# Optimization experiments

Hardware: AMD Instinct MI355X
Metric: run time of the kernel (lower is better)

Reference implementation:

```python
import jax, jax.numpy as jnp
import numpy as np
import math

NUM_HEADS = 16


def _alibi_slopes(num_heads: int):
    # geometric sequence for power-of-2 head counts (paper's scheme)
    def slopes_pow2(n):
        start = 2.0 ** (-(2.0 ** (-(math.log2(n) - 3))))
        return [start * (start ** i) for i in range(n)]
    if math.log2(num_heads).is_integer():
        return slopes_pow2(num_heads)
    c = 2 ** math.floor(math.log2(num_heads))
    extra = slopes_pow2(2 * c)[0::2][: num_heads - c]
    return slopes_pow2(c) + extra


def setup_inputs() -> dict:
    key = jax.random.key(0)
    kq, kk, kv = jax.random.split(key, 3)
    B, H, S, D = 2, NUM_HEADS, 2048, 64
    q = jax.random.normal(kq, (B, H, S, D), dtype=jnp.float32)
    k = jax.random.normal(kk, (B, H, S, D), dtype=jnp.float32)
    v = jax.random.normal(kv, (B, H, S, D), dtype=jnp.float32)
    return {"q": q, "k": k, "v": v}


def reference(q, k, v):
    B, H, Sq, D = q.shape
    Sk = k.shape[2]
    slopes = jnp.asarray(_alibi_slopes(H), dtype=jnp.float32)  # [H]
    pos = jnp.arange(Sk)
    # abs relative positions (symmetric, non-causal) as in the source
    rel = jnp.abs(pos[None, :] - pos[:, None]).astype(jnp.float32)  # [Sk, Sk]
    alibi = -slopes[:, None, None] * rel[None, :Sq, :]  # [H, Sq, Sk]
    scores = jnp.einsum("bhqd,bhkd->bhqk", q, k) / math.sqrt(D)
    scores = scores + alibi[None]
    probs = jax.nn.softmax(scores, axis=-1)
    return jnp.einsum("bhqk,bhkd->bhqd", probs, v)
```

## Files before the change

### kernel.cpp

```cpp
#include <hip/hip_runtime.h>
#include <hip/hip_bf16.h>
#include <math.h>

typedef __bf16 bf16;
typedef __attribute__((ext_vector_type(8))) bf16 bf16x8;
typedef __attribute__((ext_vector_type(2))) bf16 bf16x2;
typedef __attribute__((ext_vector_type(16))) float f32x16;
typedef __attribute__((ext_vector_type(4))) unsigned int uint4v;

#define SQ 2048
#define DH 64
#define NH 16
#define KVT 32
#define NKVT (SQ / KVT)
#define REC 8192
#define LOG2E 1.44269504088896340736f
#define THETA 14.0f
#define NITEMS 1024
#define GRID 1024

__device__ __forceinline__ float fast_exp2(float x) {
#if __has_builtin(__builtin_amdgcn_exp2f)
    return __builtin_amdgcn_exp2f(x);
#else
    return exp2f(x);
#endif
}

__device__ __forceinline__ unsigned pkbf16(float a, float b) {
    union { bf16x2 h; unsigned u; } x;
    x.h = (bf16x2){(bf16)a, (bf16)b};
    return x.u;
}

#if __has_builtin(__builtin_amdgcn_permlane32_swap)
__device__ __forceinline__ void plswap(unsigned &a, unsigned &b) {
    typedef __attribute__((ext_vector_type(2))) unsigned int uint2v;
    uint2v r = __builtin_amdgcn_permlane32_swap(a, b, false, false);
    a = r[0]; b = r[1];
}
#else
__device__ __forceinline__ void plswap(unsigned &a, unsigned &b) {
    asm volatile("v_permlane32_swap_b32 %0, %1" : "+v"(a), "+v"(b));
}
#endif

union FragU { uint4v u; bf16x8 b; };

__global__ __launch_bounds__(256)
void alibi_prep_kernel(const float* __restrict__ K, const float* __restrict__ V,
                       char* __restrict__ W, int* __restrict__ ctr) {
    __shared__ bf16 lt[64][80];
    const int t  = threadIdx.x;
    const int s0 = blockIdx.x * 64;
    const int bh = blockIdx.y;
    if (ctr && blockIdx.x == 0 && blockIdx.y == 0 && blockIdx.z == 0 && t == 0)
        *ctr = 0;
    if (blockIdx.z == 0) {
#pragma unroll
        for (int i = 0; i < 2; ++i) {
            const int g    = i * 256 + t;
            const int tile = g >> 8;
            const int cc   = g & 255;
            const int ds   = cc >> 6;
            const int lane = cc & 63;
            const float* p = K + ((size_t)bh * SQ + s0 + tile * 32 + (lane & 31)) * DH
                               + ds * 16 + (lane >> 5) * 8;
            float4 a = *(const float4*)p, b = *(const float4*)(p + 4);
            bf16x8 pk = {(bf16)a.x,(bf16)a.y,(bf16)a.z,(bf16)a.w,
                         (bf16)b.x,(bf16)b.y,(bf16)b.z,(bf16)b.w};
            *(bf16x8*)(W + (size_t)(bh * NKVT + (s0 >> 5) + tile) * REC
                         + ds * 1024 + lane * 16) = pk;
        }
    } else {
#pragma unroll
        for (int i = 0; i < 2; ++i) {
            int idx = i * 256 + t;
            int row = idx >> 3, c8 = idx & 7;
            const float* p = V + ((size_t)bh * SQ + s0 + row) * DH + c8 * 8;
            float4 a = *(const float4*)p, b = *(const float4*)(p + 4);
            bf16 e[8] = {(bf16)a.x,(bf16)a.y,(bf16)a.z,(bf16)a.w,
                         (bf16)b.x,(bf16)b.y,(bf16)b.z,(bf16)b.w};
#pragma unroll
            for (int jj = 0; jj < 8; ++jj) lt[c8 * 8 + jj][row] = e[jj];
        }
        __syncthreads();
#pragma unroll
        for (int i = 0; i < 2; ++i) {
            const int g    = i * 256 + t;
            const int tile = g >> 8;
            const int cc   = g & 255;
            const int grp  = cc >> 6;
            const int lane = cc & 63;
            const int d    = (grp >> 1) * 32 + (lane & 31);
            const int sv   = tile * 32 + (grp & 1) * 16 + (lane >> 5) * 8;
            bf16x8 v = *(const bf16x8*)&lt[d][sv];
            *(bf16x8*)(W + (size_t)(bh * NKVT + (s0 >> 5) + tile) * REC
                         + 4096 + grp * 1024 + lane * 16) = v;
        }
    }
}

__global__ __launch_bounds__(256, 2)
void alibi_attn_kernel(const float* __restrict__ Q, const char* __restrict__ W,
                       float* __restrict__ Out, int* __restrict__ ctr) {
    __shared__ float ex[2][64][72];
    __shared__ int s_id;
    const int tid  = threadIdx.x;
    const int lane = tid & 63;
    const int par  = tid >> 6;
    const int r32  = lane & 31;
    const int hi   = lane >> 5;
    const float QSCALE = 0.125f * LOG2E;

    int next_static = blockIdx.x;

    while (true) {
        if (tid == 0) s_id = ctr ? atomicAdd(ctr, 1) : next_static;
        __syncthreads();
        const int r = s_id;
        next_static += GRID;
        if (r >= NITEMS) break;

        const int h   = 15 - (r >> 6);
        const int sub = r & 63;
        const int bh  = (sub >> 5) * NH + h;
        const int q0  = (sub & 31) * 64;

        const float slope2  = exp2f(-0.5f * (float)(h + 1)) * LOG2E;
        const float SLOPE2N = -slope2;
        const int D = (int)(THETA / slope2);
        const int a0 = q0 - D;
        const int tmin = (a0 <= 0) ? 0 : (a0 >> 5);
        const int tmax = min(NKVT - 1, (q0 + 63 + D) >> 5);

        const float* Qp = Q + (size_t)bh * SQ * DH;
        float*       Op = Out + (size_t)bh * SQ * DH;
        const char*  rec = W + (size_t)bh * NKVT * REC;

        const int qrowA = q0 + r32;
        bf16x8 qfragA[4], qfragB[4];
#pragma unroll
        for (int ds = 0; ds < 4; ++ds) {
            const float* sa = Qp + (size_t)qrowA * DH + ds * 16 + hi * 8;
            float4 a = *(const float4*)sa, b = *(const float4*)(sa + 4);
            qfragA[ds] = (bf16x8){(bf16)(a.x*QSCALE),(bf16)(a.y*QSCALE),
                                  (bf16)(a.z*QSCALE),(bf16)(a.w*QSCALE),
                                  (bf16)(b.x*QSCALE),(bf16)(b.y*QSCALE),
                                  (bf16)(b.z*QSCALE),(bf16)(b.w*QSCALE)};
            const float* sb = sa + 32 * DH;
            float4 c = *(const float4*)sb, d = *(const float4*)(sb + 4);
            qfragB[ds] = (bf16x8){(bf16)(c.x*QSCALE),(bf16)(c.y*QSCALE),
                                  (bf16)(c.z*QSCALE),(bf16)(c.w*QSCALE),
                                  (bf16)(d.x*QSCALE),(bf16)(d.y*QSCALE),
                                  (bf16)(d.z*QSCALE),(bf16)(d.w*QSCALE)};
        }

        f32x16 oaccA[2], oaccB[2];
#pragma unroll
        for (int d2 = 0; d2 < 2; ++d2)
#pragma unroll
            for (int rr = 0; rr < 16; ++rr) { oaccA[d2][rr] = 0.f; oaccB[d2][rr] = 0.f; }
        float psA[4] = {0.f,0.f,0.f,0.f}, psB[4] = {0.f,0.f,0.f,0.f};
        const float qhA = (float)(qrowA - 4 * hi);

        auto LOADF = [&](bf16x8* kf, bf16x8* vf, int tt) {
            const char* rb = rec + (size_t)tt * REC + lane * 16;
#pragma unroll
            for (int ds = 0; ds < 4; ++ds) kf[ds] = *(const bf16x8*)(rb + ds * 1024);
#pragma unroll
            for (int g = 0; g < 4; ++g)    vf[g] = *(const bf16x8*)(rb + 4096 + g * 1024);
        };

        auto COMPUTE = [&](const bf16x8* kf, const bf16x8* vf, int tt) {
            const float gq0 = qhA - (float)(tt * KVT);
#pragma unroll
            for (int qs = 0; qs < 2; ++qs) {
                const bf16x8* qf = qs ? qfragB : qfragA;
                f32x16*       oa = qs ? oaccB  : oaccA;
                float*        ps = qs ? psB    : psA;
                const float   gq = qs ? gq0 + 32.f : gq0;

                f32x16 sacc;
#pragma unroll
                for (int rr = 0; rr < 16; ++rr) sacc[rr] = 0.f;
                __builtin_amdgcn_s_setprio(1);
#pragma unroll
                for (int ds = 0; ds < 4; ++ds)
                    sacc = __builtin_amdgcn_mfma_f32_32x32x16_bf16(kf[ds], qf[ds], sacc, 0, 0, 0);
                __builtin_amdgcn_s_setprio(0);

                float p[16];
#pragma unroll
                for (int reg = 0; reg < 16; ++reg) {
                    const int krel = (reg & 3) + 8 * (reg >> 2);
                    float d = gq - (float)krel;
                    float s2 = fmaf(SLOPE2N, fabsf(d), sacc[reg]);
                    float e = fast_exp2(s2);
                    p[reg] = e;
                    ps[reg & 3] += e;
                }

                __builtin_amdgcn_s_setprio(1);
#pragma unroll
                for (int ks = 0; ks < 2; ++ks) {
                    unsigned u0 = pkbf16(p[8 * ks + 0], p[8 * ks + 1]);
                    unsigned u1 = pkbf16(p[8 * ks + 2], p[8 * ks + 3]);
                    unsigned v0 = pkbf16(p[8 * ks + 4], p[8 * ks + 5]);
                    unsigned v1 = pkbf16(p[8 * ks + 6], p[8 * ks + 7]);
                    plswap(u0, v0);
                    plswap(u1, v1);
                    FragU pf; pf.u = (uint4v){u0, u1, v0, v1};
#pragma unroll
                    for (int dblk = 0; dblk < 2; ++dblk)
                        oa[dblk] = __builtin_amdgcn_mfma_f32_32x32x16_bf16(vf[dblk * 2 + ks], pf.b, oa[dblk], 0, 0, 0);
                }
                __builtin_amdgcn_s_setprio(0);
            }
        };

        {
            bf16x8 kA[4], vA[4], kB[4], vB[4];
            int t = tmin + par;
            if (t <= tmax) {
                const int n = ((tmax - t) >> 2) + 1;
                LOADF(kA, vA, t);
                int i = 0;
                while (i + 2 <= n) {
                    LOADF(kB, vB, t + 4);
                    asm volatile("s_waitcnt vmcnt(8)" ::: "memory");
                    __builtin_amdgcn_sched_barrier(0);
                    COMPUTE(kA, vA, t);
                    if (i + 2 < n) {
                        LOADF(kA, vA, t + 8);
                        asm volatile("s_waitcnt vmcnt(8)" ::: "memory");
                    } else {
                        asm volatile("s_waitcnt vmcnt(0)" ::: "memory");
                    }
                    __builtin_amdgcn_sched_barrier(0);
                    COMPUTE(kB, vB, t + 4);
                    t += 8; i += 2;
                }
                if (i < n) {
                    asm volatile("s_waitcnt vmcnt(0)" ::: "memory");
                    __builtin_amdgcn_sched_barrier(0);
                    COMPUTE(kA, vA, t);
                }
            }
        }

        float psumA = (psA[0] + psA[1]) + (psA[2] + psA[3]);
        psumA += __shfl_xor(psumA, 32);
        float psumB = (psB[0] + psB[1]) + (psB[2] + psB[3]);
        psumB += __shfl_xor(psumB, 32);

        auto WRITE = [&](int si) {
            float* s = &ex[si][lane][0];
#pragma unroll
            for (int dblk = 0; dblk < 2; ++dblk)
#pragma unroll
                for (int g2 = 0; g2 < 4; ++g2) {
                    *(float4*)(s + dblk * 16 + g2 * 4) =
                        (float4){oaccA[dblk][4*g2+0], oaccA[dblk][4*g2+1],
                                 oaccA[dblk][4*g2+2], oaccA[dblk][4*g2+3]};
                    *(float4*)(s + 36 + dblk * 16 + g2 * 4) =
                        (float4){oaccB[dblk][4*g2+0], oaccB[dblk][4*g2+1],
                                 oaccB[dblk][4*g2+2], oaccB[dblk][4*g2+3]};
                }
            s[32] = psumA;
            s[68] = psumB;
        };
        auto ADDIN = [&](int si) {
            const float* s = &ex[si][lane][0];
#pragma unroll
            for (int dblk = 0; dblk < 2; ++dblk)
#pragma unroll
                for (int g2 = 0; g2 < 4; ++g2) {
                    float4 oa = *(const float4*)(s + dblk * 16 + g2 * 4);
                    float4 ob = *(const float4*)(s + 36 + dblk * 16 + g2 * 4);
                    oaccA[dblk][4*g2+0] += oa.x; oaccA[dblk][4*g2+1] += oa.y;
                    oaccA[dblk][4*g2+2] += oa.z; oaccA[dblk][4*g2+3] += oa.w;
                    oaccB[dblk][4*g2+0] += ob.x; oaccB[dblk][4*g2+1] += ob.y;
                    oaccB[dblk][4*g2+2] += ob.z; oaccB[dblk][4*g2+3] += ob.w;
                }
            psumA += s[32];
            psumB += s[68];
        };

        if (par & 1) WRITE(par >> 1);
        __syncthreads();
        if (!(par & 1)) ADDIN(par >> 1);
        __syncthreads();
        if (par == 2) WRITE(0);
        __syncthreads();
        if (par == 0) {
            ADDIN(0);
            const float invA = 1.f / psumA;
            const float invB = 1.f / psumB;
#pragma unroll
            for (int dblk = 0; dblk < 2; ++dblk)
#pragma unroll
                for (int g2 = 0; g2 < 4; ++g2) {
                    float4 oa = {oaccA[dblk][4*g2+0] * invA, oaccA[dblk][4*g2+1] * invA,
                                 oaccA[dblk][4*g2+2] * invA, oaccA[dblk][4*g2+3] * invA};
                    *(float4*)(Op + (size_t)qrowA * DH + dblk * 32 + g2 * 8 + hi * 4) = oa;
                    float4 ob = {oaccB[dblk][4*g2+0] * invB, oaccB[dblk][4*g2+1] * invB,
                                 oaccB[dblk][4*g2+2] * invB, oaccB[dblk][4*g2+3] * invB};
                    *(float4*)(Op + (size_t)(qrowA + 32) * DH + dblk * 32 + g2 * 8 + hi * 4) = ob;
                }
        }
    }
}

extern "C" void kernel_launch(void* const* d_in, const int* in_sizes, int n_in,
                              void* d_out, int out_size, void* d_ws, size_t ws_size,
                              hipStream_t stream) {
    const float* q = (const float*)d_in[0];
    const float* k = (const float*)d_in[1];
    const float* v = (const float*)d_in[2];
    float* out = (float*)d_out;
    char* W = (char*)d_ws;
    const size_t rec_bytes = (size_t)32 * NKVT * REC;
    int* ctr = (ws_size >= rec_bytes + 4) ? (int*)(W + rec_bytes) : nullptr;

    alibi_prep_kernel<<<dim3(SQ / 64, 2 * NH, 2), dim3(256), 0, stream>>>(k, v, W, ctr);
    alibi_attn_kernel<<<dim3(GRID), dim3(256), 0, stream>>>(q, W, out, ctr);
}
```

Measured before the change: 54.48 us.

## Partition work queue into eight XCD-local queues grouping heads per chiplet

Replaces the single global atomic work counter with eight per-XCD counters, each block picking from the queue matching blockIdx.x & 7. Each XCD gets a fixed set of (batch,head) pairs chosen to balance ALiBi-window cost, so the K/V records of those heads stay in that chiplet's L2 and are reused there. The aim is better L2 locality and less contention on one atomic counter. It relies on round-robin block-to-XCD mapping and a hand-made static balance table, and it adds a trailing __syncthreads per work item.

```diff
diff --git a/kernel.cpp b/kernel.cpp
--- a/kernel.cpp
+++ b/kernel.cpp
@@ -16,7 +16,6 @@
 #define REC 8192
 #define LOG2E 1.44269504088896340736f
 #define THETA 14.0f
-#define NITEMS 1024
 #define GRID 1024
 
 __device__ __forceinline__ float fast_exp2(float x) {
@@ -46,6 +45,13 @@
 #endif
 
 union FragU { uint4v u; bf16x8 b; };
+
+__device__ __constant__ signed char XBH[8][5] = {
+    {15, 14, -1, -1, -1}, {31, 30, -1, -1, -1},
+    {13, 10,  0, 16, -1}, {29, 26,  1, 17, -1},
+    {12,  9,  4,  2, 18}, {28, 25, 20,  3, 19},
+    {11,  8,  7,  6,  5}, {27, 24, 23, 22, 21}};
+__device__ __constant__ short XNIT[8] = {64, 64, 128, 128, 160, 160, 160, 160};
 
 __global__ __launch_bounds__(256)
 void alibi_prep_kernel(const float* __restrict__ K, const float* __restrict__ V,
@@ -54,8 +60,8 @@
     const int t  = threadIdx.x;
     const int s0 = blockIdx.x * 64;
     const int bh = blockIdx.y;
-    if (ctr && blockIdx.x == 0 && blockIdx.y == 0 && blockIdx.z == 0 && t == 0)
-        *ctr = 0;
+    if (ctr && blockIdx.x == 0 && blockIdx.y == 0 && blockIdx.z == 0 && t < 8)
+        ctr[t] = 0;
     if (blockIdx.z == 0) {
 #pragma unroll
         for (int i = 0; i < 2; ++i) {
@@ -113,19 +119,20 @@
     const int hi   = lane >> 5;
     const float QSCALE = 0.125f * LOG2E;
 
-    int next_static = blockIdx.x;
+    const int x = blockIdx.x & 7;
+    const int nit = XNIT[x];
+    int next_static = blockIdx.x >> 3;
 
     while (true) {
-        if (tid == 0) s_id = ctr ? atomicAdd(ctr, 1) : next_static;
+        if (tid == 0) s_id = ctr ? atomicAdd(&ctr[x], 1) : next_static;
         __syncthreads();
         const int r = s_id;
-        next_static += GRID;
-        if (r >= NITEMS) break;
-
-        const int h   = 15 - (r >> 6);
-        const int sub = r & 63;
-        const int bh  = (sub >> 5) * NH + h;
-        const int q0  = (sub & 31) * 64;
+        next_static += 128;
+        if (r >= nit) break;
+
+        const int bh = XBH[x][r >> 5];
+        const int q0 = (r & 31) * 64;
+        const int h  = bh & (NH - 1);
 
         const float slope2  = exp2f(-0.5f * (float)(h + 1)) * LOG2E;
         const float SLOPE2N = -slope2;
@@ -309,6 +316,7 @@
                     *(float4*)(Op + (size_t)(qrowA + 32) * DH + dblk * 32 + g2 * 8 + hi * 4) = ob;
                 }
         }
+        __syncthreads();
     }
 }
 
@@ -321,7 +329,7 @@
     float* out = (float*)d_out;
     char* W = (char*)d_ws;
     const size_t rec_bytes = (size_t)32 * NKVT * REC;
-    int* ctr = (ws_size >= rec_bytes + 4) ? (int*)(W + rec_bytes) : nullptr;
+    int* ctr = (ws_size >= rec_bytes + 8 * sizeof(int)) ? (int*)(W + rec_bytes) : nullptr;
 
     alibi_prep_kernel<<<dim3(SQ / 64, 2 * NH, 2), dim3(256), 0, stream>>>(k, v, W, ctr);
     alibi_attn_kernel<<<dim3(GRID), dim3(256), 0, stream>>>(q, W, out, ctr);
```

Result: faster. 53.24 us (-2.3%).
